# Kernel tuning notes

Hardware: AMD Instinct MI355X
Metric: run time of the kernel (lower is better)

The kernel has to match this reference:

```python
import jax, jax.numpy as jnp
import numpy as np

N = 50000
E = 400000
IN_CH = 16
HID = 64
HEADS = 4
NEG_SLOPE = 0.2


def setup_inputs() -> dict:
    key = jax.random.key(0)
    ks = jax.random.split(key, 12)
    x_dyn = jax.random.normal(ks[0], (N, IN_CH), dtype=jnp.float32)
    edge_index = jax.random.randint(ks[1], (2, E), 0, N, dtype=jnp.int64)
    s = 0.1
    # conv1: heads=HEADS, out=HID, concat=False
    W1 = jax.random.normal(ks[2], (IN_CH, HEADS * HID), dtype=jnp.float32) * s
    att_src1 = jax.random.normal(ks[3], (HEADS, HID), dtype=jnp.float32) * s
    att_dst1 = jax.random.normal(ks[4], (HEADS, HID), dtype=jnp.float32) * s
    b1 = jnp.zeros((HID,), dtype=jnp.float32)
    # conv2: heads=1, out=HID
    W2 = jax.random.normal(ks[5], (HID, 1 * HID), dtype=jnp.float32) * s
    att_src2 = jax.random.normal(ks[6], (1, HID), dtype=jnp.float32) * s
    att_dst2 = jax.random.normal(ks[7], (1, HID), dtype=jnp.float32) * s
    b2 = jnp.zeros((HID,), dtype=jnp.float32)
    return {"x_dyn": x_dyn, "edge_index": edge_index,
            "W1": W1, "att_src1": att_src1, "att_dst1": att_dst1, "b1": b1,
            "W2": W2, "att_src2": att_src2, "att_dst2": att_dst2, "b2": b2}


def gat_conv(x, src, dst, W, att_src, att_dst, bias, heads, out_ch):
    n = x.shape[0]
    h = (x @ W).reshape(n, heads, out_ch)                 # [N,H,C]
    a_src = jnp.sum(h * att_src[None], axis=-1)           # [N,H]
    a_dst = jnp.sum(h * att_dst[None], axis=-1)           # [N,H]
    e = jax.nn.leaky_relu(a_src[src] + a_dst[dst], NEG_SLOPE)  # [E,H]
    # softmax over incoming edges per destination node (stable)
    emax = jax.ops.segment_max(e, dst, num_segments=n)    # [N,H]
    ex = jnp.exp(e - emax[dst])
    denom = jax.ops.segment_sum(ex, dst, num_segments=n)  # [N,H]
    alpha = ex / (denom[dst] + 1e-16)                     # [E,H]
    msg = h[src] * alpha[:, :, None]                      # [E,H,C]
    out = jax.ops.segment_sum(msg, dst, num_segments=n)   # [N,H,C]
    return jnp.mean(out, axis=1) + bias                   # concat=False -> mean over heads


def reference(x_dyn, edge_index, W1, att_src1, att_dst1, b1, W2, att_src2, att_dst2, b2):
    n = x_dyn.shape[0]
    # PyG GATConv default: add self-loops
    loop = jnp.arange(n, dtype=edge_index.dtype)
    src = jnp.concatenate([edge_index[0], loop])
    dst = jnp.concatenate([edge_index[1], loop])
    h = jax.nn.elu(gat_conv(x_dyn, src, dst, W1, att_src1, att_dst1, b1, HEADS, HID))
    h = jax.nn.elu(gat_conv(h, src, dst, W2, att_src2, att_dst2, b2, 1, HID))
    return h
```

## Files before the change

### kernel.cpp

```cpp
#include <hip/hip_runtime.h>
#include <math.h>


typedef __attribute__((ext_vector_type(8))) short s8v;
typedef __attribute__((ext_vector_type(4))) float f4v;

__device__ __forceinline__ float leaky02(float x) { return x > 0.f ? x : 0.2f * x; }
__device__ __forceinline__ float eluf(float x) { return x > 0.f ? x : expm1f(x); }
__device__ __forceinline__ unsigned short f2bf(float f) {
    unsigned u = __float_as_uint(f);
    u += 0x7FFFu + ((u >> 16) & 1u);
    return (unsigned short)(u >> 16);
}
__device__ __forceinline__ float bf2f(unsigned short h) {
    return __uint_as_float((unsigned)h << 16);
}


__global__ void k_deg_prep(const int* __restrict__ dst, int* __restrict__ deg,
                           int* __restrict__ rank, int e_cnt,
                           const float* __restrict__ x, const float* __restrict__ W1,
                           const float* __restrict__ W2,
                           unsigned short* __restrict__ xb,
                           unsigned short* __restrict__ w1catT,
                           unsigned short* __restrict__ w2tb, int n16) {
    int i = blockIdx.x * 256 + threadIdx.x;
    if (i < 4096) {
        int c = i >> 6, k = i & 63;
        w2tb[c * 64 + k] = f2bf(W2[k * 64 + c]);
        int r = i & 63;
        int h = r >> 4, k2 = r & 15;
        w1catT[c * 64 + r] = f2bf(0.25f * W1[k2 * 256 + h * 64 + c]);
    }
    if (i < n16) xb[i] = f2bf(x[i]);
    if (i < e_cnt) rank[i] = atomicAdd(&deg[dst[i]], 1);
}

__global__ void k_scan_bsums(const int* __restrict__ deg, int* __restrict__ bsum, int n) {
    __shared__ int part[4];
    int i = blockIdx.x * 256 + threadIdx.x;
    int v = (i < n) ? deg[i] : 0;
    int w = v;
#pragma unroll
    for (int off = 32; off; off >>= 1) w += __shfl_xor(w, off, 64);
    if ((threadIdx.x & 63) == 0) part[threadIdx.x >> 6] = w;
    __syncthreads();
    if (threadIdx.x == 0) bsum[blockIdx.x] = part[0] + part[1] + part[2] + part[3];
}

__global__ void k_scan_final(const int* __restrict__ deg, const int* __restrict__ bsum,
                             int* __restrict__ off, int n, int e_cnt, int nb) {
    __shared__ int pre[256];
    __shared__ int s[256];
    int t = threadIdx.x;
    pre[t] = (t < nb && t < (int)blockIdx.x) ? bsum[t] : 0;
    __syncthreads();
#pragma unroll
    for (int d = 128; d; d >>= 1) {
        if (t < d) pre[t] += pre[t + d];
        __syncthreads();
    }
    int bofs = pre[0];
    int i = blockIdx.x * 256 + t;
    int v = (i < n) ? deg[i] : 0;
    s[t] = v;
    __syncthreads();
#pragma unroll
    for (int d = 1; d < 256; d <<= 1) {
        int add = (t >= d) ? s[t - d] : 0;
        __syncthreads();
        s[t] += add;
        __syncthreads();
    }
    int o = bofs + s[t] - v;
    if (i < n) off[i] = o;
    if (i == 0) off[n] = e_cnt;
}


__global__ void k1s_scores(const float* __restrict__ x, const float* __restrict__ W1,
                           const float* __restrict__ attS, const float* __restrict__ attD,
                           float* __restrict__ a_src1, float* __restrict__ a_dst1,
                           int n_nodes) {
    __shared__ float wS[64], wD[64];
    int t = threadIdx.x;
    if (t < 64) {
        int h = t >> 4, k = t & 15;
        float s = 0.f, d = 0.f;
        for (int c = 0; c < 64; ++c) {
            float w = W1[k * 256 + h * 64 + c];
            s += w * attS[h * 64 + c];
            d += w * attD[h * 64 + c];
        }
        wS[t] = s; wD[t] = d;
    }
    __syncthreads();
    int i = blockIdx.x * 256 + t;
    if (i >= n_nodes * 4) return;
    int n = i >> 2, h = i & 3;
    const float4* xr = (const float4*)(x + (size_t)n * 16);
    const float* ws = wS + h * 16;
    const float* wd = wD + h * 16;
    float s = 0.f, d = 0.f;
#pragma unroll
    for (int q = 0; q < 4; ++q) {
        float4 xv = xr[q];
        s += xv.x * ws[4 * q] + xv.y * ws[4 * q + 1] + xv.z * ws[4 * q + 2] + xv.w * ws[4 * q + 3];
        d += xv.x * wd[4 * q] + xv.y * wd[4 * q + 1] + xv.z * wd[4 * q + 2] + xv.w * wd[4 * q + 3];
    }
    a_src1[i] = s;
    a_dst1[i] = d;
}

__global__ void k3_scatter(const int* __restrict__ src, const int* __restrict__ dst,
                           const float* __restrict__ a_src1, const float* __restrict__ a_dst1,
                           const int* __restrict__ off, const int* __restrict__ rank,
                           int* __restrict__ csr_src, float4* __restrict__ csr_ex, int e_cnt) {
    int e = blockIdx.x * blockDim.x + threadIdx.x;
    if (e >= e_cnt) return;
    int s = src[e], d = dst[e];
    float4 as = *(const float4*)(a_src1 + (size_t)s * 4);
    float4 ad = *(const float4*)(a_dst1 + (size_t)d * 4);
    float4 ex;
    ex.x = expf(leaky02(as.x + ad.x));
    ex.y = expf(leaky02(as.y + ad.y));
    ex.z = expf(leaky02(as.z + ad.z));
    ex.w = expf(leaky02(as.w + ad.w));
    int pos = off[d] + rank[e];
    csr_src[pos] = s;
    csr_ex[pos] = ex;
}

__global__ void __launch_bounds__(256, 6)
k4a_xagg(const int* __restrict__ off, const int* __restrict__ csr_src,
         const float4* __restrict__ csr_ex, const unsigned short* __restrict__ xb,
         const float* __restrict__ a_src1, const float* __restrict__ a_dst1,
         unsigned short* __restrict__ xaggb, int n_nodes) {
    __shared__ int   sS[4][16];
    __shared__ float eS[4][64];
    const int wave = threadIdx.x >> 6, lane = threadIdx.x & 63;
    const int head = lane >> 4, k = lane & 15;
    for (int n = blockIdx.x * 4 + wave; n < n_nodes; n += gridDim.x * 4) {
        int beg = off[n], end = off[n + 1];
        float se = expf(leaky02(a_src1[n * 4 + head] + a_dst1[n * 4 + head]));
        float den = se;
        float agg = se * bf2f(xb[(size_t)n * 16 + k]);
        for (int base = beg; base < end; base += 16) {
            int m = end - base; if (m > 16) m = 16;
            if (lane < m) {
                sS[wave][lane] = csr_src[base + lane];
                ((float4*)eS[wave])[lane] = csr_ex[base + lane];
            }
            int i = 0;
            for (; i + 8 <= m; i += 8) {
                int s0 = sS[wave][i];     float e0 = eS[wave][4 * i + head];
                int s1 = sS[wave][i + 1]; float e1 = eS[wave][4 * (i + 1) + head];
                int s2 = sS[wave][i + 2]; float e2 = eS[wave][4 * (i + 2) + head];
                int s3 = sS[wave][i + 3]; float e3 = eS[wave][4 * (i + 3) + head];
                int s4 = sS[wave][i + 4]; float e4 = eS[wave][4 * (i + 4) + head];
                int s5 = sS[wave][i + 5]; float e5 = eS[wave][4 * (i + 5) + head];
                int s6 = sS[wave][i + 6]; float e6 = eS[wave][4 * (i + 6) + head];
                int s7 = sS[wave][i + 7]; float e7 = eS[wave][4 * (i + 7) + head];
                float v0 = bf2f(xb[(size_t)s0 * 16 + k]);
                float v1 = bf2f(xb[(size_t)s1 * 16 + k]);
                float v2 = bf2f(xb[(size_t)s2 * 16 + k]);
                float v3 = bf2f(xb[(size_t)s3 * 16 + k]);
                float v4 = bf2f(xb[(size_t)s4 * 16 + k]);
                float v5 = bf2f(xb[(size_t)s5 * 16 + k]);
                float v6 = bf2f(xb[(size_t)s6 * 16 + k]);
                float v7 = bf2f(xb[(size_t)s7 * 16 + k]);
                agg += e0 * v0 + e1 * v1 + e2 * v2 + e3 * v3
                     + e4 * v4 + e5 * v5 + e6 * v6 + e7 * v7;
                den += e0 + e1 + e2 + e3 + e4 + e5 + e6 + e7;
            }
            for (; i < m; ++i) {
                int s = sS[wave][i];
                float eh = eS[wave][4 * i + head];
                agg += eh * bf2f(xb[(size_t)s * 16 + k]);
                den += eh;
            }
        }
        xaggb[(size_t)n * 64 + lane] = f2bf(agg / (den + 1e-16f));
    }
}

__global__ void __launch_bounds__(256)
k5_mlp(const unsigned short* __restrict__ xaggb, const unsigned short* __restrict__ w1catT,
       const unsigned short* __restrict__ w2tb, const float* __restrict__ b1,
       const float* __restrict__ attS2, const float* __restrict__ attD2,
       unsigned short* __restrict__ h2b, float* __restrict__ a_src2,
       float* __restrict__ a_dst2, int n_nodes) {
    __shared__ unsigned short x2s[16 * 72];
    __shared__ float psS[4][16], pdS[4][16];
    const int wave = threadIdx.x >> 6, lane = threadIdx.x & 63;
    const int quad = lane >> 4, l16 = lane & 15;
    const int c = wave * 16 + l16;
    const int base = blockIdx.x * 16;
    int arow = base + l16; if (arow >= n_nodes) arow = n_nodes - 1;
    const s8v a0 = *(const s8v*)(xaggb + (size_t)arow * 64 + quad * 8);
    const s8v a1f = *(const s8v*)(xaggb + (size_t)arow * 64 + 32 + quad * 8);
    const s8v c0 = *(const s8v*)(w1catT + c * 64 + quad * 8);
    const s8v c1 = *(const s8v*)(w1catT + c * 64 + 32 + quad * 8);
    f4v acc = {0.f, 0.f, 0.f, 0.f};
    acc = __builtin_amdgcn_mfma_f32_16x16x32_bf16(a0, c0, acc, 0, 0, 0);
    acc = __builtin_amdgcn_mfma_f32_16x16x32_bf16(a1f, c1, acc, 0, 0, 0);
    float b1c = b1[c];
#pragma unroll
    for (int r = 0; r < 4; ++r)
        x2s[(quad * 4 + r) * 72 + c] = f2bf(eluf(acc[r] + b1c));
    __syncthreads();
    const s8v b0 = *(const s8v*)(w2tb + c * 64 + quad * 8);
    const s8v b1v = *(const s8v*)(w2tb + c * 64 + 32 + quad * 8);
    const s8v a2_0 = *(const s8v*)(x2s + l16 * 72 + quad * 8);
    const s8v a2_1 = *(const s8v*)(x2s + l16 * 72 + 32 + quad * 8);
    f4v acc2 = {0.f, 0.f, 0.f, 0.f};
    acc2 = __builtin_amdgcn_mfma_f32_16x16x32_bf16(a2_0, b0, acc2, 0, 0, 0);
    acc2 = __builtin_amdgcn_mfma_f32_16x16x32_bf16(a2_1, b1v, acc2, 0, 0, 0);
    const float attS_c = attS2[c], attD_c = attD2[c];
    float pS[4], pD[4];
#pragma unroll
    for (int r = 0; r < 4; ++r) {
        int node = base + quad * 4 + r;
        if (node < n_nodes) h2b[(size_t)node * 64 + c] = f2bf(acc2[r]);
        pS[r] = acc2[r] * attS_c;
        pD[r] = acc2[r] * attD_c;
    }
#pragma unroll
    for (int mask = 1; mask < 16; mask <<= 1) {
#pragma unroll
        for (int r = 0; r < 4; ++r) {
            pS[r] += __shfl_xor(pS[r], mask, 64);
            pD[r] += __shfl_xor(pD[r], mask, 64);
        }
    }
    if (l16 == 0) {
#pragma unroll
        for (int r = 0; r < 4; ++r) {
            psS[wave][quad * 4 + r] = pS[r];
            pdS[wave][quad * 4 + r] = pD[r];
        }
    }
    __syncthreads();
    if (threadIdx.x < 16) {
        int node = base + threadIdx.x;
        if (node < n_nodes) {
            a_src2[node] = psS[0][threadIdx.x] + psS[1][threadIdx.x] +
                           psS[2][threadIdx.x] + psS[3][threadIdx.x];
            a_dst2[node] = pdS[0][threadIdx.x] + pdS[1][threadIdx.x] +
                           pdS[2][threadIdx.x] + pdS[3][threadIdx.x];
        }
    }
}


__global__ void __launch_bounds__(256, 6)
k8_agg2(const int* __restrict__ off, const int* __restrict__ csr_src,
        const unsigned short* __restrict__ h2b,
        const float* __restrict__ a_src2, const float* __restrict__ a_dst2,
        const float* __restrict__ b2, float* __restrict__ out, int n_nodes) {
    __shared__ int   sS[4][64];
    __shared__ float eS[4][64];
    const int wave = threadIdx.x >> 6, lane = threadIdx.x & 63;
    const int g = lane >> 4, l16 = lane & 15;
    const float4 b2v = ((const float4*)b2)[l16];
    for (int n = blockIdx.x * 4 + wave; n < n_nodes; n += gridDim.x * 4) {
        int beg = off[n], end = off[n + 1];
        float adn = a_dst2[n];
        float se = expf(leaky02(a_src2[n] + adn));
        ushort4 qs = ((const ushort4*)(h2b + (size_t)n * 64))[l16];
        float w0 = (g == 0) ? se : 0.f;
        float a0 = w0 * bf2f(qs.x), a1 = w0 * bf2f(qs.y);
        float a2 = w0 * bf2f(qs.z), a3 = w0 * bf2f(qs.w);
        float den = w0;
        for (int base = beg; base < end; base += 64) {
            int m = end - base; if (m > 64) m = 64;
            if (lane < m) {
                int s = csr_src[base + lane];
                sS[wave][lane] = s;
                eS[wave][lane] = expf(leaky02(a_src2[s] + adn));
            }
            int i = g;
            for (; i + 12 < m; i += 16) {
                int s0 = sS[wave][i];
                int s1 = sS[wave][i + 4];
                int s2 = sS[wave][i + 8];
                int s3 = sS[wave][i + 12];
                ushort4 q0 = ((const ushort4*)(h2b + (size_t)s0 * 64))[l16];
                ushort4 q1 = ((const ushort4*)(h2b + (size_t)s1 * 64))[l16];
                ushort4 q2 = ((const ushort4*)(h2b + (size_t)s2 * 64))[l16];
                ushort4 q3 = ((const ushort4*)(h2b + (size_t)s3 * 64))[l16];
                float e0 = eS[wave][i];
                float e1 = eS[wave][i + 4];
                float e2 = eS[wave][i + 8];
                float e3 = eS[wave][i + 12];
                a0 += e0 * bf2f(q0.x) + e1 * bf2f(q1.x) + e2 * bf2f(q2.x) + e3 * bf2f(q3.x);
                a1 += e0 * bf2f(q0.y) + e1 * bf2f(q1.y) + e2 * bf2f(q2.y) + e3 * bf2f(q3.y);
                a2 += e0 * bf2f(q0.z) + e1 * bf2f(q1.z) + e2 * bf2f(q2.z) + e3 * bf2f(q3.z);
                a3 += e0 * bf2f(q0.w) + e1 * bf2f(q1.w) + e2 * bf2f(q2.w) + e3 * bf2f(q3.w);
                den += e0 + e1 + e2 + e3;
            }
            for (; i < m; i += 4) {
                int s = sS[wave][i];
                float eh = eS[wave][i];
                ushort4 q = ((const ushort4*)(h2b + (size_t)s * 64))[l16];
                a0 += eh * bf2f(q.x); a1 += eh * bf2f(q.y);
                a2 += eh * bf2f(q.z); a3 += eh * bf2f(q.w);
                den += eh;
            }
        }
        a0 += __shfl_xor(a0, 16, 64); a0 += __shfl_xor(a0, 32, 64);
        a1 += __shfl_xor(a1, 16, 64); a1 += __shfl_xor(a1, 32, 64);
        a2 += __shfl_xor(a2, 16, 64); a2 += __shfl_xor(a2, 32, 64);
        a3 += __shfl_xor(a3, 16, 64); a3 += __shfl_xor(a3, 32, 64);
        den += __shfl_xor(den, 16, 64); den += __shfl_xor(den, 32, 64);
        if (lane < 16) {
            float inv = 1.f / (den + 1e-16f);
            float4 ov;
            ov.x = eluf(a0 * inv + b2v.x);
            ov.y = eluf(a1 * inv + b2v.y);
            ov.z = eluf(a2 * inv + b2v.z);
            ov.w = eluf(a3 * inv + b2v.w);
            ((float4*)(out + (size_t)n * 64))[l16] = ov;
        }
    }
}

extern "C" void kernel_launch(void* const* d_in, const int* in_sizes, int n_in,
                              void* d_out, int out_size, void* d_ws, size_t ws_size,
                              hipStream_t stream) {
    const float* x   = (const float*)d_in[0];
    const int*   ei  = (const int*)d_in[1];
    const float* W1  = (const float*)d_in[2];
    const float* as1 = (const float*)d_in[3];
    const float* ad1 = (const float*)d_in[4];
    const float* b1  = (const float*)d_in[5];
    const float* W2  = (const float*)d_in[6];
    const float* as2 = (const float*)d_in[7];
    const float* ad2 = (const float*)d_in[8];
    const float* b2  = (const float*)d_in[9];
    float* out = (float*)d_out;

    const int n = in_sizes[0] / 16;
    const int e = in_sizes[1] / 2;
    const int* src = ei;
    const int* dst = ei + e;
    const int nb = (n + 255) / 256;

    float* ws = (float*)d_ws;
    size_t o = 0;
    float4* csr_ex  = (float4*)(ws + o); o += (size_t)e * 4;
    unsigned short* xb    = (unsigned short*)(ws + o); o += (size_t)n * 8;
    unsigned short* xaggb = (unsigned short*)(ws + o); o += (size_t)n * 32;
    unsigned short* w2tb   = (unsigned short*)(ws + o); o += 2048;
    unsigned short* w1catT = (unsigned short*)(ws + o); o += 2048;
    float*  a_src1  = ws + o; o += (size_t)n * 4;
    float*  a_dst1  = ws + o; o += (size_t)n * 4;
    unsigned short* h2b = (unsigned short*)(ws + o); o += (size_t)n * 32;
    float*  a_src2  = ws + o; o += (size_t)n;
    float*  a_dst2  = ws + o; o += (size_t)n;
    int*    csr_src = (int*)(ws + o); o += (size_t)e;
    int*    rank    = (int*)(ws + o); o += (size_t)e;
    int*    deg     = (int*)(ws + o); o += (size_t)n;
    int*    off     = (int*)(ws + o); o += (size_t)(n + 4);
    int*    bsum    = (int*)(ws + o); o += 256;

    hipMemsetAsync(deg, 0, (size_t)n * sizeof(int), stream);

    const int prep_threads = (n * 16 > e) ? n * 16 : e;
    k_deg_prep<<<(prep_threads + 255) / 256, 256, 0, stream>>>(
        dst, deg, rank, e, x, W1, W2, xb, w1catT, w2tb, n * 16);
    k1s_scores<<<(n * 4 + 255) / 256, 256, 0, stream>>>(x, W1, as1, ad1, a_src1, a_dst1, n);
    k_scan_bsums<<<nb, 256, 0, stream>>>(deg, bsum, n);
    k_scan_final<<<nb, 256, 0, stream>>>(deg, bsum, off, n, e, nb);

    k3_scatter<<<(e + 255) / 256, 256, 0, stream>>>(src, dst, a_src1, a_dst1, off, rank,
                                                    csr_src, csr_ex, e);
    k4a_xagg<<<(n + 3) / 4, 256, 0, stream>>>(off, csr_src, csr_ex, xb, a_src1, a_dst1,
                                              xaggb, n);
    k5_mlp<<<(n + 15) / 16, 256, 0, stream>>>(xaggb, w1catT, w2tb, b1, as2, ad2,
                                              h2b, a_src2, a_dst2, n);

    k8_agg2<<<(n + 3) / 4, 256, 0, stream>>>(off, csr_src, h2b, a_src2, a_dst2, b2, out, n);
}
```

Measured before the change: 182.3 us.

## Fuse layer-1 aggregation with MLP kernel and fold score computation into prep

```diff
diff --git a/kernel.cpp b/kernel.cpp
--- a/kernel.cpp
+++ b/kernel.cpp
@@ -21,10 +21,15 @@
                            int* __restrict__ rank, int e_cnt,
                            const float* __restrict__ x, const float* __restrict__ W1,
                            const float* __restrict__ W2,
+                           const float* __restrict__ attS, const float* __restrict__ attD,
                            unsigned short* __restrict__ xb,
                            unsigned short* __restrict__ w1catT,
-                           unsigned short* __restrict__ w2tb, int n16) {
-    int i = blockIdx.x * 256 + threadIdx.x;
+                           unsigned short* __restrict__ w2tb,
+                           float* __restrict__ a_src1, float* __restrict__ a_dst1,
+                           int n16, int n4) {
+    __shared__ float wS[64], wD[64];
+    int t = threadIdx.x;
+    int i = blockIdx.x * 256 + t;
     if (i < 4096) {
         int c = i >> 6, k = i & 63;
         w2tb[c * 64 + k] = f2bf(W2[k * 64 + c]);
@@ -34,6 +39,34 @@
     }
     if (i < n16) xb[i] = f2bf(x[i]);
     if (i < e_cnt) rank[i] = atomicAdd(&deg[dst[i]], 1);
+    if ((int)blockIdx.x * 256 < n4) {
+        if (t < 64) {
+            int h = t >> 4, k = t & 15;
+            float s = 0.f, d = 0.f;
+            for (int c = 0; c < 64; ++c) {
+                float w = W1[k * 256 + h * 64 + c];
+                s += w * attS[h * 64 + c];
+                d += w * attD[h * 64 + c];
+            }
+            wS[t] = s; wD[t] = d;
+        }
+        __syncthreads();
+        if (i < n4) {
+            int n = i >> 2, h = i & 3;
+            const float4* xr = (const float4*)(x + (size_t)n * 16);
+            const float* ws = wS + h * 16;
+            const float* wd = wD + h * 16;
+            float s = 0.f, d = 0.f;
+#pragma unroll
+            for (int q = 0; q < 4; ++q) {
+                float4 xv = xr[q];
+                s += xv.x * ws[4 * q] + xv.y * ws[4 * q + 1] + xv.z * ws[4 * q + 2] + xv.w * ws[4 * q + 3];
+                d += xv.x * wd[4 * q] + xv.y * wd[4 * q + 1] + xv.z * wd[4 * q + 2] + xv.w * wd[4 * q + 3];
+            }
+            a_src1[i] = s;
+            a_dst1[i] = d;
+        }
+    }
 }
 
 __global__ void k_scan_bsums(const int* __restrict__ deg, int* __restrict__ bsum, int n) {
@@ -75,41 +108,6 @@
     int o = bofs + s[t] - v;
     if (i < n) off[i] = o;
     if (i == 0) off[n] = e_cnt;
-}
-
-
-__global__ void k1s_scores(const float* __restrict__ x, const float* __restrict__ W1,
-                           const float* __restrict__ attS, const float* __restrict__ attD,
-                           float* __restrict__ a_src1, float* __restrict__ a_dst1,
-                           int n_nodes) {
-    __shared__ float wS[64], wD[64];
-    int t = threadIdx.x;
-    if (t < 64) {
-        int h = t >> 4, k = t & 15;
-        float s = 0.f, d = 0.f;
-        for (int c = 0; c < 64; ++c) {
-            float w = W1[k * 256 + h * 64 + c];
-            s += w * attS[h * 64 + c];
-            d += w * attD[h * 64 + c];
-        }
-        wS[t] = s; wD[t] = d;
-    }
-    __syncthreads();
-    int i = blockIdx.x * 256 + t;
-    if (i >= n_nodes * 4) return;
-    int n = i >> 2, h = i & 3;
-    const float4* xr = (const float4*)(x + (size_t)n * 16);
-    const float* ws = wS + h * 16;
-    const float* wd = wD + h * 16;
-    float s = 0.f, d = 0.f;
-#pragma unroll
-    for (int q = 0; q < 4; ++q) {
-        float4 xv = xr[q];
-        s += xv.x * ws[4 * q] + xv.y * ws[4 * q + 1] + xv.z * ws[4 * q + 2] + xv.w * ws[4 * q + 3];
-        d += xv.x * wd[4 * q] + xv.y * wd[4 * q + 1] + xv.z * wd[4 * q + 2] + xv.w * wd[4 * q + 3];
-    }
-    a_src1[i] = s;
-    a_dst1[i] = d;
 }
 
 __global__ void k3_scatter(const int* __restrict__ src, const int* __restrict__ dst,
@@ -131,74 +129,74 @@
     csr_ex[pos] = ex;
 }
 
-__global__ void __launch_bounds__(256, 6)
-k4a_xagg(const int* __restrict__ off, const int* __restrict__ csr_src,
-         const float4* __restrict__ csr_ex, const unsigned short* __restrict__ xb,
-         const float* __restrict__ a_src1, const float* __restrict__ a_dst1,
-         unsigned short* __restrict__ xaggb, int n_nodes) {
+__global__ void __launch_bounds__(256)
+k45_agg_mlp(const int* __restrict__ off, const int* __restrict__ csr_src,
+            const float4* __restrict__ csr_ex, const unsigned short* __restrict__ xb,
+            const float* __restrict__ a_src1, const float* __restrict__ a_dst1,
+            const unsigned short* __restrict__ w1catT, const unsigned short* __restrict__ w2tb,
+            const float* __restrict__ b1, const float* __restrict__ attS2,
+            const float* __restrict__ attD2, unsigned short* __restrict__ h2b,
+            float* __restrict__ a_src2, float* __restrict__ a_dst2, int n_nodes) {
+    __shared__ unsigned short xaggS[16 * 72];
+    __shared__ unsigned short x2s[16 * 72];
     __shared__ int   sS[4][16];
     __shared__ float eS[4][64];
+    __shared__ float psS[4][16], pdS[4][16];
     const int wave = threadIdx.x >> 6, lane = threadIdx.x & 63;
     const int head = lane >> 4, k = lane & 15;
-    for (int n = blockIdx.x * 4 + wave; n < n_nodes; n += gridDim.x * 4) {
-        int beg = off[n], end = off[n + 1];
-        float se = expf(leaky02(a_src1[n * 4 + head] + a_dst1[n * 4 + head]));
-        float den = se;
-        float agg = se * bf2f(xb[(size_t)n * 16 + k]);
-        for (int base = beg; base < end; base += 16) {
-            int m = end - base; if (m > 16) m = 16;
-            if (lane < m) {
-                sS[wave][lane] = csr_src[base + lane];
-                ((float4*)eS[wave])[lane] = csr_ex[base + lane];
-            }
-            int i = 0;
-            for (; i + 8 <= m; i += 8) {
-                int s0 = sS[wave][i];     float e0 = eS[wave][4 * i + head];
-                int s1 = sS[wave][i + 1]; float e1 = eS[wave][4 * (i + 1) + head];
-                int s2 = sS[wave][i + 2]; float e2 = eS[wave][4 * (i + 2) + head];
-                int s3 = sS[wave][i + 3]; float e3 = eS[wave][4 * (i + 3) + head];
-                int s4 = sS[wave][i + 4]; float e4 = eS[wave][4 * (i + 4) + head];
-                int s5 = sS[wave][i + 5]; float e5 = eS[wave][4 * (i + 5) + head];
-                int s6 = sS[wave][i + 6]; float e6 = eS[wave][4 * (i + 6) + head];
-                int s7 = sS[wave][i + 7]; float e7 = eS[wave][4 * (i + 7) + head];
-                float v0 = bf2f(xb[(size_t)s0 * 16 + k]);
-                float v1 = bf2f(xb[(size_t)s1 * 16 + k]);
-                float v2 = bf2f(xb[(size_t)s2 * 16 + k]);
-                float v3 = bf2f(xb[(size_t)s3 * 16 + k]);
-                float v4 = bf2f(xb[(size_t)s4 * 16 + k]);
-                float v5 = bf2f(xb[(size_t)s5 * 16 + k]);
-                float v6 = bf2f(xb[(size_t)s6 * 16 + k]);
-                float v7 = bf2f(xb[(size_t)s7 * 16 + k]);
-                agg += e0 * v0 + e1 * v1 + e2 * v2 + e3 * v3
-                     + e4 * v4 + e5 * v5 + e6 * v6 + e7 * v7;
-                den += e0 + e1 + e2 + e3 + e4 + e5 + e6 + e7;
-            }
-            for (; i < m; ++i) {
-                int s = sS[wave][i];
-                float eh = eS[wave][4 * i + head];
-                agg += eh * bf2f(xb[(size_t)s * 16 + k]);
-                den += eh;
-            }
-        }
-        xaggb[(size_t)n * 64 + lane] = f2bf(agg / (den + 1e-16f));
-    }
-}
-
-__global__ void __launch_bounds__(256)
-k5_mlp(const unsigned short* __restrict__ xaggb, const unsigned short* __restrict__ w1catT,
-       const unsigned short* __restrict__ w2tb, const float* __restrict__ b1,
-       const float* __restrict__ attS2, const float* __restrict__ attD2,
-       unsigned short* __restrict__ h2b, float* __restrict__ a_src2,
-       float* __restrict__ a_dst2, int n_nodes) {
-    __shared__ unsigned short x2s[16 * 72];
-    __shared__ float psS[4][16], pdS[4][16];
-    const int wave = threadIdx.x >> 6, lane = threadIdx.x & 63;
+    const int base = blockIdx.x * 16;
+#pragma unroll 1
+    for (int r = 0; r < 4; ++r) {
+        int n = base + wave * 4 + r;
+        float agg = 0.f, den = 1e-16f;
+        if (n < n_nodes) {
+            int beg = off[n], end = off[n + 1];
+            float se = expf(leaky02(a_src1[n * 4 + head] + a_dst1[n * 4 + head]));
+            den += se;
+            agg = se * bf2f(xb[(size_t)n * 16 + k]);
+            for (int cb = beg; cb < end; cb += 16) {
+                int m = end - cb; if (m > 16) m = 16;
+                if (lane < m) {
+                    sS[wave][lane] = csr_src[cb + lane];
+                    ((float4*)eS[wave])[lane] = csr_ex[cb + lane];
+                }
+                int i = 0;
+                for (; i + 8 <= m; i += 8) {
+                    int s0 = sS[wave][i];     float e0 = eS[wave][4 * i + head];
+                    int s1 = sS[wave][i + 1]; float e1 = eS[wave][4 * (i + 1) + head];
+                    int s2 = sS[wave][i + 2]; float e2 = eS[wave][4 * (i + 2) + head];
+                    int s3 = sS[wave][i + 3]; float e3 = eS[wave][4 * (i + 3) + head];
+                    int s4 = sS[wave][i + 4]; float e4 = eS[wave][4 * (i + 4) + head];
+                    int s5 = sS[wave][i + 5]; float e5 = eS[wave][4 * (i + 5) + head];
+                    int s6 = sS[wave][i + 6]; float e6 = eS[wave][4 * (i + 6) + head];
+                    int s7 = sS[wave][i + 7]; float e7 = eS[wave][4 * (i + 7) + head];
+                    float v0 = bf2f(xb[(size_t)s0 * 16 + k]);
+                    float v1 = bf2f(xb[(size_t)s1 * 16 + k]);
+                    float v2 = bf2f(xb[(size_t)s2 * 16 + k]);
+                    float v3 = bf2f(xb[(size_t)s3 * 16 + k]);
+                    float v4 = bf2f(xb[(size_t)s4 * 16 + k]);
+                    float v5 = bf2f(xb[(size_t)s5 * 16 + k]);
+                    float v6 = bf2f(xb[(size_t)s6 * 16 + k]);
+                    float v7 = bf2f(xb[(size_t)s7 * 16 + k]);
+                    agg += e0 * v0 + e1 * v1 + e2 * v2 + e3 * v3
+                         + e4 * v4 + e5 * v5 + e6 * v6 + e7 * v7;
+                    den += e0 + e1 + e2 + e3 + e4 + e5 + e6 + e7;
+                }
+                for (; i < m; ++i) {
+                    int s = sS[wave][i];
+                    float eh = eS[wave][4 * i + head];
+                    agg += eh * bf2f(xb[(size_t)s * 16 + k]);
+                    den += eh;
+                }
+            }
+        }
+        xaggS[(wave * 4 + r) * 72 + lane] = f2bf(agg / den);
+    }
+    __syncthreads();
     const int quad = lane >> 4, l16 = lane & 15;
     const int c = wave * 16 + l16;
-    const int base = blockIdx.x * 16;
-    int arow = base + l16; if (arow >= n_nodes) arow = n_nodes - 1;
-    const s8v a0 = *(const s8v*)(xaggb + (size_t)arow * 64 + quad * 8);
-    const s8v a1f = *(const s8v*)(xaggb + (size_t)arow * 64 + 32 + quad * 8);
+    const s8v a0 = *(const s8v*)(xaggS + l16 * 72 + quad * 8);
+    const s8v a1f = *(const s8v*)(xaggS + l16 * 72 + 32 + quad * 8);
     const s8v c0 = *(const s8v*)(w1catT + c * 64 + quad * 8);
     const s8v c1 = *(const s8v*)(w1catT + c * 64 + 32 + quad * 8);
     f4v acc = {0.f, 0.f, 0.f, 0.f};
@@ -350,7 +348,6 @@
     size_t o = 0;
     float4* csr_ex  = (float4*)(ws + o); o += (size_t)e * 4;
     unsigned short* xb    = (unsigned short*)(ws + o); o += (size_t)n * 8;
-    unsigned short* xaggb = (unsigned short*)(ws + o); o += (size_t)n * 32;
     unsigned short* w2tb   = (unsigned short*)(ws + o); o += 2048;
     unsigned short* w1catT = (unsigned short*)(ws + o); o += 2048;
     float*  a_src1  = ws + o; o += (size_t)n * 4;
@@ -368,17 +365,16 @@
 
     const int prep_threads = (n * 16 > e) ? n * 16 : e;
     k_deg_prep<<<(prep_threads + 255) / 256, 256, 0, stream>>>(
-        dst, deg, rank, e, x, W1, W2, xb, w1catT, w2tb, n * 16);
-    k1s_scores<<<(n * 4 + 255) / 256, 256, 0, stream>>>(x, W1, as1, ad1, a_src1, a_dst1, n);
+        dst, deg, rank, e, x, W1, W2, as1, ad1, xb, w1catT, w2tb,
+        a_src1, a_dst1, n * 16, n * 4);
     k_scan_bsums<<<nb, 256, 0, stream>>>(deg, bsum, n);
     k_scan_final<<<nb, 256, 0, stream>>>(deg, bsum, off, n, e, nb);
 
     k3_scatter<<<(e + 255) / 256, 256, 0, stream>>>(src, dst, a_src1, a_dst1, off, rank,
                                                     csr_src, csr_ex, e);
-    k4a_xagg<<<(n + 3) / 4, 256, 0, stream>>>(off, csr_src, csr_ex, xb, a_src1, a_dst1,
-                                              xaggb, n);
-    k5_mlp<<<(n + 15) / 16, 256, 0, stream>>>(xaggb, w1catT, w2tb, b1, as2, ad2,
-                                              h2b, a_src2, a_dst2, n);
+    k45_agg_mlp<<<(n + 15) / 16, 256, 0, stream>>>(off, csr_src, csr_ex, xb,
+                                                   a_src1, a_dst1, w1catT, w2tb, b1,
+                                                   as2, ad2, h2b, a_src2, a_dst2, n);
 
     k8_agg2<<<(n + 3) / 4, 256, 0, stream>>>(off, csr_src, h2b, a_src2, a_dst2, b2, out, n);
 }
```

Measured after the change: 176.9 us. -3.0%, faster.
